# Optimization experiments

Measured on AMD Instinct MI355X. Metric: run time of the kernel, lower is better.

The kernel has to match this reference:

```python
import jax, jax.numpy as jnp
import numpy as np

B, S, D = 2, 2048, 1024
H, HD = 16, 64          # num_heads, head_dim
W = 16                  # window_size; band half-width = W // 2 = 8


def setup_inputs() -> dict:
    key = jax.random.key(0)
    ks = jax.random.split(key, 5)
    std = 0.02
    inp = {
        'hidden_states': jax.random.normal(ks[0], (B, S, D), dtype=jnp.float32),
        'Wq': jax.random.normal(ks[1], (D, D), dtype=jnp.float32) * std,
        'Wk': jax.random.normal(ks[2], (D, D), dtype=jnp.float32) * std,
        'Wv': jax.random.normal(ks[3], (D, D), dtype=jnp.float32) * std,
        'Wo': jax.random.normal(ks[4], (D, D), dtype=jnp.float32) * std,
        'bq': jnp.zeros((D,), dtype=jnp.float32),
        'bk': jnp.zeros((D,), dtype=jnp.float32),
        'bv': jnp.zeros((D,), dtype=jnp.float32),
        'bo': jnp.zeros((D,), dtype=jnp.float32),
    }
    return inp


def reference(hidden_states, Wq, bq, Wk, bk, Wv, bv, Wo, bo):
    # Projections (y = x @ W + b)
    q = hidden_states @ Wq + bq   # [B,S,D]
    k = hidden_states @ Wk + bk
    v = hidden_states @ Wv + bv
    # Split heads -> [B,H,S,HD]
    q = q.reshape(B, S, H, HD).transpose(0, 2, 1, 3)
    k = k.reshape(B, S, H, HD).transpose(0, 2, 1, 3)
    v = v.reshape(B, S, H, HD).transpose(0, 2, 1, 3)
    # Band mask: original fills scores for j in [i - W//2, i + W//2]
    idx = jnp.arange(S)
    band = jnp.abs(idx[:, None] - idx[None, :]) <= (W // 2)   # [S,S]
    scores = jnp.einsum('bhsd,bhtd->bhst', q, k) / jnp.sqrt(jnp.float32(HD))
    # Faithful to source: out-of-band entries stay 0.0 (NOT -inf),
    # and softmax runs over the FULL row, so exp(0)=1 contributions remain.
    scores = jnp.where(band[None, None], scores, 0.0)
    attn = jax.nn.softmax(scores, axis=-1)                    # [B,H,S,S]
    ctx = jnp.einsum('bhst,bhtd->bhsd', attn, v)              # [B,H,S,HD]
    ctx = ctx.transpose(0, 2, 1, 3).reshape(B, S, D)
    return ctx @ Wo + bo
```

## Files before the change

### kernel.cpp

```cpp
#include <hip/hip_runtime.h>
#include <hip/hip_bf16.h>
#include <cmath>

#define S_LEN 2048
#define DMODEL 1024
#define NH 16
#define HD_DIM 64

typedef __bf16 bf16;
typedef __bf16 bf16x2 __attribute__((ext_vector_type(2)));
typedef __bf16 bf16x8 __attribute__((ext_vector_type(8)));
typedef float f32x4 __attribute__((ext_vector_type(4)));

__global__ __launch_bounds__(256) void prep_all(const float* __restrict__ x,
                                                const float* __restrict__ Wq,
                                                const float* __restrict__ Wk,
                                                const float* __restrict__ Wv,
                                                const float* __restrict__ Wo,
                                                const float* __restrict__ bq,
                                                const float* __restrict__ bk,
                                                const float* __restrict__ bv,
                                                bf16* __restrict__ xb,
                                                bf16* __restrict__ wtall,
                                                bf16* __restrict__ wot,
                                                float* __restrict__ ball,
                                                float* __restrict__ vsm) {
    __shared__ float tile[64][65];
    const int bid = blockIdx.x;
    const int tid = threadIdx.x;
    if (bid < 2048) {
        int i = (bid * 256 + tid) * 8;
        float4 v0 = *(const float4*)(x + i);
        float4 v1 = *(const float4*)(x + i + 4);
        bf16x8 o;
        o[0] = (bf16)v0.x; o[1] = (bf16)v0.y; o[2] = (bf16)v0.z; o[3] = (bf16)v0.w;
        o[4] = (bf16)v1.x; o[5] = (bf16)v1.y; o[6] = (bf16)v1.z; o[7] = (bf16)v1.w;
        *(bf16x8*)(xb + i) = o;
    } else if (bid < 3072) {
        int t = bid - 2048;
        int z = t >> 8;
        t &= 255;
        const float* W = (z == 0) ? Wq : (z == 1) ? Wk : (z == 2) ? Wv : Wo;
        bf16* Wt = (z == 3) ? wot : wtall + (size_t)z * 1048576;
        int n0 = (t & 15) * 64, k0 = (t >> 4) * 64;
        int tr = tid >> 6, tc = tid & 63;
#pragma unroll
        for (int i = 0; i < 16; ++i) {
            int r = tr + i * 4;
            tile[r][tc] = W[(size_t)(k0 + r) * DMODEL + n0 + tc];
        }
        __syncthreads();
#pragma unroll
        for (int i = 0; i < 16; ++i) {
            int r = tr + i * 4;
            Wt[(size_t)(n0 + r) * DMODEL + k0 + tc] = (bf16)tile[tc][r];
        }
    } else {
        int i = (bid - 3072) * 256 + tid;
        float v = (i < 1024) ? bq[i] : (i < 2048) ? bk[i - 1024] : bv[i - 2048];
        ball[i] = v;
        if (i >= 2048) {
            int c = i - 2048;
            vsm[c]        = 2048.0f * v;
            vsm[1024 + c] = 2048.0f * v;
        }
    }
}

__device__ __forceinline__ void gload_lds16(const void* g, void* l) {
    __builtin_amdgcn_global_load_lds((const __attribute__((address_space(1))) void*)g,
                                     (__attribute__((address_space(3))) void*)l, 16, 0, 0);
}

#define BAR() asm volatile("s_barrier" ::: "memory")
#define VMC(N) asm volatile("s_waitcnt vmcnt(" #N ")" ::: "memory")

#define QST(T, D) do {                                                                 \
    _Pragma("unroll") for (int _p = 0; _p < 4; ++_p)                                   \
        gload_lds16(aSrc + (size_t)(32 * _p) * KDIM + (size_t)(T) * 64,                \
                    aDstW + (D) * 16384 + _p * 4096);                                  \
    _Pragma("unroll") for (int _p = 0; _p < 6; ++_p)                                   \
        gload_lds16(bSrc + (size_t)(32 * _p) * KDIM + (size_t)(T) * 64,                \
                    bDstW + (D) * 24576 + _p * 4096);                                  \
} while (0)

template <int KDIM>
__global__ __launch_bounds__(256, 2) void gemm_qkv(const bf16* __restrict__ A,
                                                   const bf16* __restrict__ Bt,
                                                   bf16* __restrict__ C,
                                                   const float* __restrict__ bias,
                                                   float* __restrict__ vsm,
                                                   int N) {
    __shared__ bf16 smem[40960];
    char* sc = (char*)smem;

    const int tid  = threadIdx.x;
    const int wv   = tid >> 6;
    const int lane = tid & 63;
    const int ll   = lane & 15;
    const int kh   = lane >> 4;
    const int wm   = wv >> 1;
    const int wn   = wv & 1;

    const int flat = blockIdx.y * 32 + blockIdx.x;
    const int L    = (flat & 7) * 64 + (flat >> 3);
    const int m0   = ((L & 63) >> 1) * 128;
    const int n0   = ((L >> 6) * 2 + (L & 1)) * 192;

    const int swcol = (((tid & 7) ^ ((tid >> 3) & 7)) << 3);
    const bf16* aSrc = A + (size_t)(m0 + (tid >> 3)) * KDIM + swcol;
    const bf16* bSrc = Bt + (size_t)(n0 + (tid >> 3)) * KDIM + swcol;
    char* aDstW = sc + wv * 1024;
    char* bDstW = sc + 32768 + wv * 1024;

    const int aBase = wm * 8192 + ll * 128;
    const int bBase = (wn * 96 + ll) * 128;
    const int ks0 = ((kh ^ (ll & 7)) << 4);
    const int ks1 = (((4 | kh) ^ (ll & 7)) << 4);

    f32x4 acc[4][6] = {};

    constexpr int NT = KDIM / 64;

    QST(0, 0);
    VMC(0); BAR();

#pragma unroll 1
    for (int t = 0; t < NT; ++t) {
        const int d = t & 1;
        if (t + 1 < NT) QST(t + 1, d ^ 1);

        bf16x8 a[4][2], b[3][2];
#pragma unroll
        for (int mf = 0; mf < 4; ++mf) {
            a[mf][0] = *(const bf16x8*)(sc + d * 16384 + aBase + mf * 2048 + ks0);
            a[mf][1] = *(const bf16x8*)(sc + d * 16384 + aBase + mf * 2048 + ks1);
        }
#pragma unroll
        for (int nf = 0; nf < 3; ++nf) {
            b[nf][0] = *(const bf16x8*)(sc + 32768 + d * 24576 + bBase + nf * 2048 + ks0);
            b[nf][1] = *(const bf16x8*)(sc + 32768 + d * 24576 + bBase + nf * 2048 + ks1);
        }
        __builtin_amdgcn_s_setprio(1);
#pragma unroll
        for (int mf = 0; mf < 4; ++mf)
#pragma unroll
            for (int nf = 0; nf < 3; ++nf)
#pragma unroll
                for (int k = 0; k < 2; ++k)
                    acc[mf][nf] = __builtin_amdgcn_mfma_f32_16x16x32_bf16(
                        a[mf][k], b[nf][k], acc[mf][nf], 0, 0, 0);
        __builtin_amdgcn_s_setprio(0);
#pragma unroll
        for (int nf = 0; nf < 3; ++nf) {
            b[nf][0] = *(const bf16x8*)(sc + 32768 + d * 24576 + bBase + (nf + 3) * 2048 + ks0);
            b[nf][1] = *(const bf16x8*)(sc + 32768 + d * 24576 + bBase + (nf + 3) * 2048 + ks1);
        }
        __builtin_amdgcn_s_setprio(1);
#pragma unroll
        for (int mf = 0; mf < 4; ++mf)
#pragma unroll
            for (int nf = 0; nf < 3; ++nf)
#pragma unroll
                for (int k = 0; k < 2; ++k)
                    acc[mf][nf + 3] = __builtin_amdgcn_mfma_f32_16x16x32_bf16(
                        a[mf][k], b[nf][k], acc[mf][nf + 3], 0, 0, 0);
        __builtin_amdgcn_s_setprio(0);

        VMC(0); BAR();
    }

#pragma unroll
    for (int nf = 0; nf < 6; ++nf) {
        const int col = n0 + wn * 96 + nf * 16 + ll;
        const float bv_ = bias[col];
#pragma unroll
        for (int mf = 0; mf < 4; ++mf) {
            const int row = m0 + wm * 64 + mf * 16 + kh * 4;
#pragma unroll
            for (int r = 0; r < 4; ++r)
                C[(size_t)(row + r) * N + col] = (bf16)(acc[mf][nf][r] + bv_);
        }
    }

    {
        const int bidx = m0 >> 11;
#pragma unroll
        for (int nf = 0; nf < 6; ++nf) {
            if (n0 + wn * 96 + nf * 16 >= 2048) {
                float p = 0.f;
#pragma unroll
                for (int mf = 0; mf < 4; ++mf)
#pragma unroll
                    for (int r = 0; r < 4; ++r) p += acc[mf][nf][r];
                p += __shfl_xor(p, 16);
                p += __shfl_xor(p, 32);
                if (kh == 0)
                    atomicAdd(vsm + bidx * 1024 + (n0 + wn * 96 + nf * 16 + ll - 2048), p);
            }
        }
    }
}

#define OST(T, D) do {                                                                 \
    _Pragma("unroll") for (int _p = 0; _p < 2; ++_p)                                   \
        gload_lds16(aSrc + (size_t)(32 * _p) * 1024 + (size_t)(T) * 64,                \
                    aDstW + (D) * 8192 + _p * 4096);                                   \
    _Pragma("unroll") for (int _p = 0; _p < 4; ++_p)                                   \
        gload_lds16(bSrc + (size_t)(32 * _p) * 1024 + (size_t)(T) * 64,                \
                    bDstW + (D) * 16384 + _p * 4096);                                  \
} while (0)

__global__ __launch_bounds__(256, 2) void gemm_bt(const bf16* __restrict__ A,
                                                  const bf16* __restrict__ Bt,
                                                  float* __restrict__ C,
                                                  const float* __restrict__ bias,
                                                  int N, int K) {
    __shared__ bf16 smem[24576];
    char* sc = (char*)smem;
    const int tid  = threadIdx.x;
    const int wv   = tid >> 6;
    const int lane = tid & 63;
    const int ll   = lane & 15;
    const int kh   = lane >> 4;
    const int wm   = wv >> 1;
    const int wn   = wv & 1;

    const int flat = blockIdx.y * 64 + blockIdx.x;
    const int L    = (flat & 7) * 64 + (flat >> 3);
    const int m0   = (L & 63) * 64;
    const int n0   = (L >> 6) * 128;

    const int swcol = (((tid & 7) ^ ((tid >> 3) & 7)) << 3);
    const bf16* aSrc = A + (size_t)(m0 + (tid >> 3)) * 1024 + swcol;
    const bf16* bSrc = Bt + (size_t)(n0 + (tid >> 3)) * 1024 + swcol;
    char* aDstW = sc + wv * 1024;
    char* bDstW = sc + 16384 + wv * 1024;

    const int aBase = wm * 4096 + ll * 128;
    const int bBase = (wn * 64 + ll) * 128;
    const int ks0 = ((kh ^ (ll & 7)) << 4);
    const int ks1 = (((4 | kh) ^ (ll & 7)) << 4);

    f32x4 acc[2][4] = {};
    const int NT = K / 64;

    OST(0, 0);
    VMC(0); BAR();

#pragma unroll 1
    for (int t = 0; t < NT; ++t) {
        const int d = t & 1;
        if (t + 1 < NT) OST(t + 1, d ^ 1);

        bf16x8 a[2][2], b[4][2];
#pragma unroll
        for (int mf = 0; mf < 2; ++mf) {
            a[mf][0] = *(const bf16x8*)(sc + d * 8192 + aBase + mf * 2048 + ks0);
            a[mf][1] = *(const bf16x8*)(sc + d * 8192 + aBase + mf * 2048 + ks1);
        }
#pragma unroll
        for (int nf = 0; nf < 4; ++nf) {
            b[nf][0] = *(const bf16x8*)(sc + 16384 + d * 16384 + bBase + nf * 2048 + ks0);
            b[nf][1] = *(const bf16x8*)(sc + 16384 + d * 16384 + bBase + nf * 2048 + ks1);
        }

        __builtin_amdgcn_s_setprio(1);
#pragma unroll
        for (int mf = 0; mf < 2; ++mf)
#pragma unroll
            for (int nf = 0; nf < 4; ++nf)
#pragma unroll
                for (int k = 0; k < 2; ++k)
                    acc[mf][nf] = __builtin_amdgcn_mfma_f32_16x16x32_bf16(
                        a[mf][k], b[nf][k], acc[mf][nf], 0, 0, 0);
        __builtin_amdgcn_s_setprio(0);

        VMC(0); BAR();
    }

#pragma unroll
    for (int mf = 0; mf < 2; ++mf) {
#pragma unroll
        for (int nf = 0; nf < 4; ++nf) {
            int col = n0 + wn * 64 + nf * 16 + ll;
            float bv_ = bias[col];
#pragma unroll
            for (int r = 0; r < 4; ++r) {
                int row = m0 + wm * 32 + mf * 16 + kh * 4 + r;
                C[(size_t)row * N + col] = acc[mf][nf][r] + bv_;
            }
        }
    }
}

__global__ __launch_bounds__(256) void band_attn(const bf16* __restrict__ qkv,
                                                 const float* __restrict__ vsum,
                                                 bf16* __restrict__ ctx) {
    int bid = blockIdx.x;
    int it = bid & 31;
    int h  = (bid >> 5) & 15;
    int b  = bid >> 9;
    const int i0 = it * 64;

    __shared__ bf16 qs[64 * 72];
    __shared__ bf16 ks[80 * 72];
    __shared__ bf16 vs[80 * 72];
    __shared__ float wsc[64 * 19];
    __shared__ float wsum[64];

    int tid = threadIdx.x;

    for (int idx = tid; idx < 64 * 8; idx += 256) {
        int r = idx >> 3, c = idx & 7;
        size_t g = (size_t)(b * S_LEN + i0 + r) * 3072 + h * 64 + c * 8;
        *(int4*)&qs[r * 72 + c * 8] = *(const int4*)&qkv[g];
    }
    for (int idx = tid; idx < 80 * 8; idx += 256) {
        int r = idx >> 3, c = idx & 7;
        int j = i0 - 8 + r;
        int4 kv = {0, 0, 0, 0}, vv = {0, 0, 0, 0};
        if (j >= 0 && j < S_LEN) {
            size_t base = (size_t)(b * S_LEN + j) * 3072 + h * 64 + c * 8;
            kv = *(const int4*)&qkv[base + 1024];
            vv = *(const int4*)&qkv[base + 2048];
        }
        *(int4*)&ks[r * 72 + c * 8] = kv;
        *(int4*)&vs[r * 72 + c * 8] = vv;
    }
    __syncthreads();

    {
        int i = tid >> 2, jg = tid & 3;
        bf16x8 qv[8];
#pragma unroll
        for (int c = 0; c < 8; ++c) qv[c] = *(const bf16x8*)&qs[i * 72 + c * 8];
        for (int jj = jg; jj < 17; jj += 4) {
            int j = i0 + i - 8 + jj;
            float w = 0.f;
            if (j >= 0 && j < S_LEN) {
                float dot = 0.f;
#pragma unroll
                for (int c = 0; c < 8; ++c) {
                    bf16x8 kv = *(const bf16x8*)&ks[(i + jj) * 72 + c * 8];
#pragma unroll
                    for (int e = 0; e < 8; ++e) dot += (float)qv[c][e] * (float)kv[e];
                }
                w = expm1f(dot * 0.125f);
            }
            wsc[i * 19 + jj] = w;
        }
    }
    __syncthreads();
    if (tid < 64) {
        float s = 0.f;
#pragma unroll
        for (int jj = 0; jj < 17; ++jj) s += wsc[tid * 19 + jj];
        wsum[tid] = s + (float)S_LEN;
    }
    __syncthreads();

    {
        int d0 = (tid & 7) * 8, ig = tid >> 3;
        const float* vbp = vsum + (b * NH + h) * HD_DIM + d0;
        float vb[8];
#pragma unroll
        for (int e = 0; e < 8; ++e) vb[e] = vbp[e];
        for (int i = ig; i < 64; i += 32) {
            float a[8];
#pragma unroll
            for (int e = 0; e < 8; ++e) a[e] = vb[e];
#pragma unroll
            for (int jj = 0; jj < 17; ++jj) {
                float w = wsc[i * 19 + jj];
                bf16x8 pv = *(const bf16x8*)&vs[(i + jj) * 72 + d0];
#pragma unroll
                for (int e = 0; e < 8; ++e) a[e] += w * (float)pv[e];
            }
            float inv = 1.0f / wsum[i];
            bf16x8 st;
#pragma unroll
            for (int e = 0; e < 8; ++e) st[e] = (bf16)(a[e] * inv);
            *(bf16x8*)&ctx[(size_t)(b * S_LEN + i0 + i) * 1024 + h * 64 + d0] = st;
        }
    }
}

extern "C" void kernel_launch(void* const* d_in, const int* in_sizes, int n_in,
                              void* d_out, int out_size, void* d_ws, size_t ws_size,
                              hipStream_t stream) {
    const float* x  = (const float*)d_in[0];
    const float* Wq = (const float*)d_in[1];
    const float* Wk = (const float*)d_in[2];
    const float* Wv = (const float*)d_in[3];
    const float* Wo = (const float*)d_in[4];
    const float* bq = (const float*)d_in[5];
    const float* bk = (const float*)d_in[6];
    const float* bv = (const float*)d_in[7];
    const float* bo = (const float*)d_in[8];

    char* ws = (char*)d_ws;
    bf16*  xb    = (bf16*)(ws);
    bf16*  wtall = (bf16*)(ws + 8388608);
    bf16*  wot   = (bf16*)(ws + 14680064);
    float* ball  = (float*)(ws + 16777216);
    bf16*  qkv   = (bf16*)(ws + 16789504);
    bf16*  ctxb  = (bf16*)(ws + 41955328);
    float* vsm   = (float*)(ws + 50343936);

    prep_all<<<3084, 256, 0, stream>>>(x, Wq, Wk, Wv, Wo, bq, bk, bv,
                                       xb, wtall, wot, ball, vsm);

    gemm_qkv<1024><<<dim3(32, 16), 256, 0, stream>>>(xb, wtall, qkv, ball, vsm, 3072);

    band_attn<<<1024, 256, 0, stream>>>(qkv, vsm, ctxb);

    gemm_bt<<<dim3(64, 8), 256, 0, stream>>>(ctxb, wot, (float*)d_out, bo, 1024, 1024);
}
```

Measured before the change: 71.11 us.

## Quantize QKV projection inputs to FP8 and compute V column sums separately

```diff
diff --git a/kernel.cpp b/kernel.cpp
--- a/kernel.cpp
+++ b/kernel.cpp
@@ -8,7 +8,7 @@
 #define HD_DIM 64
 
 typedef __bf16 bf16;
-typedef __bf16 bf16x2 __attribute__((ext_vector_type(2)));
+typedef unsigned char u8;
 typedef __bf16 bf16x8 __attribute__((ext_vector_type(8)));
 typedef float f32x4 __attribute__((ext_vector_type(4)));
 
@@ -20,51 +20,80 @@
                                                 const float* __restrict__ bq,
                                                 const float* __restrict__ bk,
                                                 const float* __restrict__ bv,
-                                                bf16* __restrict__ xb,
-                                                bf16* __restrict__ wtall,
+                                                u8* __restrict__ x8,
+                                                u8* __restrict__ wt8,
                                                 bf16* __restrict__ wot,
                                                 float* __restrict__ ball,
-                                                float* __restrict__ vsm) {
+                                                float* __restrict__ vpart) {
     __shared__ float tile[64][65];
     const int bid = blockIdx.x;
     const int tid = threadIdx.x;
-    if (bid < 2048) {
-        int i = (bid * 256 + tid) * 8;
-        float4 v0 = *(const float4*)(x + i);
-        float4 v1 = *(const float4*)(x + i + 4);
-        bf16x8 o;
-        o[0] = (bf16)v0.x; o[1] = (bf16)v0.y; o[2] = (bf16)v0.z; o[3] = (bf16)v0.w;
-        o[4] = (bf16)v1.x; o[5] = (bf16)v1.y; o[6] = (bf16)v1.z; o[7] = (bf16)v1.w;
-        *(bf16x8*)(xb + i) = o;
-    } else if (bid < 3072) {
-        int t = bid - 2048;
-        int z = t >> 8;
+    if (bid < 512) {
+        const int r0 = bid * 8, c0 = tid * 4;
+        float s0 = 0.f, s1 = 0.f, s2 = 0.f, s3 = 0.f;
+#pragma unroll
+        for (int r = 0; r < 8; ++r) {
+            float4 v = *(const float4*)(x + (size_t)(r0 + r) * 1024 + c0);
+            int pk = __builtin_amdgcn_cvt_pk_fp8_f32(v.x, v.y, 0, false);
+            pk = __builtin_amdgcn_cvt_pk_fp8_f32(v.z, v.w, pk, true);
+            *(int*)(x8 + (size_t)(r0 + r) * 1024 + c0) = pk;
+            s0 += v.x; s1 += v.y; s2 += v.z; s3 += v.w;
+        }
+        float4 st = {s0, s1, s2, s3};
+        *(float4*)(vpart + (size_t)bid * 1024 + c0) = st;
+    } else if (bid < 1536) {
+        int t = bid - 512;
+        const int z = t >> 8;
         t &= 255;
         const float* W = (z == 0) ? Wq : (z == 1) ? Wk : (z == 2) ? Wv : Wo;
-        bf16* Wt = (z == 3) ? wot : wtall + (size_t)z * 1048576;
-        int n0 = (t & 15) * 64, k0 = (t >> 4) * 64;
-        int tr = tid >> 6, tc = tid & 63;
+        const int n0 = (t & 15) * 64, k0 = (t >> 4) * 64;
+        const int tr = tid >> 6, tc = tid & 63;
 #pragma unroll
         for (int i = 0; i < 16; ++i) {
             int r = tr + i * 4;
             tile[r][tc] = W[(size_t)(k0 + r) * DMODEL + n0 + tc];
         }
         __syncthreads();
-#pragma unroll
-        for (int i = 0; i < 16; ++i) {
-            int r = tr + i * 4;
-            Wt[(size_t)(n0 + r) * DMODEL + k0 + tc] = (bf16)tile[tc][r];
+        if (z < 3) {
+            u8* Wt = wt8 + (size_t)z * 1048576;
+#pragma unroll
+            for (int i = 0; i < 16; ++i) {
+                int r = tr + i * 4;
+                int pk = __builtin_amdgcn_cvt_pk_fp8_f32(tile[tc][r] * 16.f,
+                                                         0.f, 0, false);
+                Wt[(size_t)(n0 + r) * DMODEL + k0 + tc] = (u8)(pk & 0xff);
+            }
+        } else {
+#pragma unroll
+            for (int i = 0; i < 16; ++i) {
+                int r = tr + i * 4;
+                wot[(size_t)(n0 + r) * DMODEL + k0 + tc] = (bf16)tile[tc][r];
+            }
         }
     } else {
-        int i = (bid - 3072) * 256 + tid;
-        float v = (i < 1024) ? bq[i] : (i < 2048) ? bk[i - 1024] : bv[i - 2048];
-        ball[i] = v;
-        if (i >= 2048) {
-            int c = i - 2048;
-            vsm[c]        = 2048.0f * v;
-            vsm[1024 + c] = 2048.0f * v;
-        }
-    }
+        int i = (bid - 1536) * 256 + tid;
+        ball[i] = (i < 1024) ? bq[i] : (i < 2048) ? bk[i - 1024] : bv[i - 2048];
+    }
+}
+
+__global__ void xsum_final(const float* __restrict__ vpart, float* __restrict__ xsum) {
+    int idx = blockIdx.x * 256 + threadIdx.x;
+    int b = idx >> 10, c = idx & 1023;
+    float s = 0.f;
+#pragma unroll 8
+    for (int i = 0; i < 256; ++i) s += vpart[(size_t)(b * 256 + i) * 1024 + c];
+    xsum[idx] = s;
+}
+
+__global__ void vsm_gemm(const float* __restrict__ xsum, const float* __restrict__ Wv,
+                         const float* __restrict__ bv, float* __restrict__ vsm) {
+    int idx = blockIdx.x * 256 + threadIdx.x;
+    int b = idx >> 10, n = idx & 1023;
+    float acc = 2048.0f * bv[n];
+    const float* xs = xsum + b * 1024;
+#pragma unroll 8
+    for (int k = 0; k < 1024; ++k) acc += xs[k] * Wv[(size_t)k * 1024 + n];
+    vsm[idx] = acc;
 }
 
 __device__ __forceinline__ void gload_lds16(const void* g, void* l) {
@@ -75,24 +104,21 @@
 #define BAR() asm volatile("s_barrier" ::: "memory")
 #define VMC(N) asm volatile("s_waitcnt vmcnt(" #N ")" ::: "memory")
 
-#define QST(T, D) do {                                                                 \
+#define QST8(T, D) do {                                                                \
     _Pragma("unroll") for (int _p = 0; _p < 4; ++_p)                                   \
-        gload_lds16(aSrc + (size_t)(32 * _p) * KDIM + (size_t)(T) * 64,                \
+        gload_lds16(aSrc + (size_t)(32 * _p) * 1024 + (size_t)(T) * 128,               \
                     aDstW + (D) * 16384 + _p * 4096);                                  \
     _Pragma("unroll") for (int _p = 0; _p < 6; ++_p)                                   \
-        gload_lds16(bSrc + (size_t)(32 * _p) * KDIM + (size_t)(T) * 64,                \
+        gload_lds16(bSrc + (size_t)(32 * _p) * 1024 + (size_t)(T) * 128,               \
                     bDstW + (D) * 24576 + _p * 4096);                                  \
 } while (0)
 
-template <int KDIM>
-__global__ __launch_bounds__(256, 2) void gemm_qkv(const bf16* __restrict__ A,
-                                                   const bf16* __restrict__ Bt,
-                                                   bf16* __restrict__ C,
-                                                   const float* __restrict__ bias,
-                                                   float* __restrict__ vsm,
-                                                   int N) {
-    __shared__ bf16 smem[40960];
-    char* sc = (char*)smem;
+__global__ __launch_bounds__(256, 2) void gemm_qkv8(const u8* __restrict__ A,
+                                                    const u8* __restrict__ Bt,
+                                                    bf16* __restrict__ C,
+                                                    const float* __restrict__ bias,
+                                                    int N) {
+    __shared__ char sc[81920];
 
     const int tid  = threadIdx.x;
     const int wv   = tid >> 6;
@@ -107,65 +133,47 @@
     const int m0   = ((L & 63) >> 1) * 128;
     const int n0   = ((L >> 6) * 2 + (L & 1)) * 192;
 
-    const int swcol = (((tid & 7) ^ ((tid >> 3) & 7)) << 3);
-    const bf16* aSrc = A + (size_t)(m0 + (tid >> 3)) * KDIM + swcol;
-    const bf16* bSrc = Bt + (size_t)(n0 + (tid >> 3)) * KDIM + swcol;
+    const int swb = (((tid & 7) ^ ((tid >> 3) & 7)) << 4);
+    const char* aSrc = (const char*)A + (size_t)(m0 + (tid >> 3)) * 1024 + swb;
+    const char* bSrc = (const char*)Bt + (size_t)(n0 + (tid >> 3)) * 1024 + swb;
     char* aDstW = sc + wv * 1024;
     char* bDstW = sc + 32768 + wv * 1024;
 
     const int aBase = wm * 8192 + ll * 128;
     const int bBase = (wn * 96 + ll) * 128;
-    const int ks0 = ((kh ^ (ll & 7)) << 4);
-    const int ks1 = (((4 | kh) ^ (ll & 7)) << 4);
+    const int sw16 = (ll & 7) << 4;
 
     f32x4 acc[4][6] = {};
 
-    constexpr int NT = KDIM / 64;
-
-    QST(0, 0);
+    constexpr int NT = 8;
+
+    QST8(0, 0);
     VMC(0); BAR();
 
 #pragma unroll 1
     for (int t = 0; t < NT; ++t) {
         const int d = t & 1;
-        if (t + 1 < NT) QST(t + 1, d ^ 1);
-
-        bf16x8 a[4][2], b[3][2];
-#pragma unroll
-        for (int mf = 0; mf < 4; ++mf) {
-            a[mf][0] = *(const bf16x8*)(sc + d * 16384 + aBase + mf * 2048 + ks0);
-            a[mf][1] = *(const bf16x8*)(sc + d * 16384 + aBase + mf * 2048 + ks1);
-        }
-#pragma unroll
-        for (int nf = 0; nf < 3; ++nf) {
-            b[nf][0] = *(const bf16x8*)(sc + 32768 + d * 24576 + bBase + nf * 2048 + ks0);
-            b[nf][1] = *(const bf16x8*)(sc + 32768 + d * 24576 + bBase + nf * 2048 + ks1);
-        }
-        __builtin_amdgcn_s_setprio(1);
-#pragma unroll
-        for (int mf = 0; mf < 4; ++mf)
-#pragma unroll
-            for (int nf = 0; nf < 3; ++nf)
-#pragma unroll
-                for (int k = 0; k < 2; ++k)
-                    acc[mf][nf] = __builtin_amdgcn_mfma_f32_16x16x32_bf16(
-                        a[mf][k], b[nf][k], acc[mf][nf], 0, 0, 0);
-        __builtin_amdgcn_s_setprio(0);
-#pragma unroll
-        for (int nf = 0; nf < 3; ++nf) {
-            b[nf][0] = *(const bf16x8*)(sc + 32768 + d * 24576 + bBase + (nf + 3) * 2048 + ks0);
-            b[nf][1] = *(const bf16x8*)(sc + 32768 + d * 24576 + bBase + (nf + 3) * 2048 + ks1);
-        }
-        __builtin_amdgcn_s_setprio(1);
-#pragma unroll
-        for (int mf = 0; mf < 4; ++mf)
-#pragma unroll
-            for (int nf = 0; nf < 3; ++nf)
-#pragma unroll
-                for (int k = 0; k < 2; ++k)
-                    acc[mf][nf + 3] = __builtin_amdgcn_mfma_f32_16x16x32_bf16(
-                        a[mf][k], b[nf][k], acc[mf][nf + 3], 0, 0, 0);
-        __builtin_amdgcn_s_setprio(0);
+        if (t + 1 < NT) QST8(t + 1, d ^ 1);
+
+#pragma unroll
+        for (int ks = 0; ks < 4; ++ks) {
+            const int akb = ((ks * 32 + kh * 8) ^ sw16);
+            long a[4], b[6];
+#pragma unroll
+            for (int mf = 0; mf < 4; ++mf)
+                a[mf] = *(const long*)(sc + d * 16384 + aBase + mf * 2048 + akb);
+#pragma unroll
+            for (int nf = 0; nf < 6; ++nf)
+                b[nf] = *(const long*)(sc + 32768 + d * 24576 + bBase + nf * 2048 + akb);
+            __builtin_amdgcn_s_setprio(1);
+#pragma unroll
+            for (int mf = 0; mf < 4; ++mf)
+#pragma unroll
+                for (int nf = 0; nf < 6; ++nf)
+                    acc[mf][nf] = __builtin_amdgcn_mfma_f32_16x16x32_fp8_fp8(
+                        a[mf], b[nf], acc[mf][nf], 0, 0, 0);
+            __builtin_amdgcn_s_setprio(0);
+        }
 
         VMC(0); BAR();
     }
@@ -179,25 +187,7 @@
             const int row = m0 + wm * 64 + mf * 16 + kh * 4;
 #pragma unroll
             for (int r = 0; r < 4; ++r)
-                C[(size_t)(row + r) * N + col] = (bf16)(acc[mf][nf][r] + bv_);
-        }
-    }
-
-    {
-        const int bidx = m0 >> 11;
-#pragma unroll
-        for (int nf = 0; nf < 6; ++nf) {
-            if (n0 + wn * 96 + nf * 16 >= 2048) {
-                float p = 0.f;
-#pragma unroll
-                for (int mf = 0; mf < 4; ++mf)
-#pragma unroll
-                    for (int r = 0; r < 4; ++r) p += acc[mf][nf][r];
-                p += __shfl_xor(p, 16);
-                p += __shfl_xor(p, 32);
-                if (kh == 0)
-                    atomicAdd(vsm + bidx * 1024 + (n0 + wn * 96 + nf * 16 + ll - 2048), p);
-            }
+                C[(size_t)(row + r) * N + col] = (bf16)(acc[mf][nf][r] * 0.0625f + bv_);
         }
     }
 }
@@ -400,18 +390,22 @@
     const float* bo = (const float*)d_in[8];
 
     char* ws = (char*)d_ws;
-    bf16*  xb    = (bf16*)(ws);
-    bf16*  wtall = (bf16*)(ws + 8388608);
-    bf16*  wot   = (bf16*)(ws + 14680064);
-    float* ball  = (float*)(ws + 16777216);
-    bf16*  qkv   = (bf16*)(ws + 16789504);
-    bf16*  ctxb  = (bf16*)(ws + 41955328);
-    float* vsm   = (float*)(ws + 50343936);
-
-    prep_all<<<3084, 256, 0, stream>>>(x, Wq, Wk, Wv, Wo, bq, bk, bv,
-                                       xb, wtall, wot, ball, vsm);
-
-    gemm_qkv<1024><<<dim3(32, 16), 256, 0, stream>>>(xb, wtall, qkv, ball, vsm, 3072);
+    u8*    x8    = (u8*)(ws);
+    u8*    wt8   = (u8*)(ws + 4194304);
+    bf16*  wot   = (bf16*)(ws + 7340032);
+    float* ball  = (float*)(ws + 9437184);
+    float* xsum  = (float*)(ws + 9453568);
+    float* vsm   = (float*)(ws + 9461760);
+    float* vpart = (float*)(ws + 9469952);
+    bf16*  qkv   = (bf16*)(ws + 11567104);
+    bf16*  ctxb  = (bf16*)(ws + 36732928);
+
+    prep_all<<<1548, 256, 0, stream>>>(x, Wq, Wk, Wv, Wo, bq, bk, bv,
+                                       x8, wt8, wot, ball, vpart);
+    xsum_final<<<8, 256, 0, stream>>>(vpart, xsum);
+    vsm_gemm<<<8, 256, 0, stream>>>(xsum, Wv, bv, vsm);
+
+    gemm_qkv8<<<dim3(32, 16), 256, 0, stream>>>(x8, wt8, qkv, ball, 3072);
 
     band_attn<<<1024, 256, 0, stream>>>(qkv, vsm, ctxb);
 
```

New measurement: 131.1 us, median of 2. 84.4% more time.
